# Kernel optimization log

Hardware: AMD Instinct MI355X
Metric: run time of the kernel (lower is better)

Reference implementation:

```python
import jax, jax.numpy as jnp
import numpy as np

N_HEADS = 16

def _apply_rope(x, cos, sin):
    # x: [B, S, H, D]; cos/sin: [S, D//2]
    B, S, H, D = x.shape
    half = D // 2
    x1, x2 = x[..., :half], x[..., half:]
    c = cos[:S, None, :]  # [S, 1, half] -> broadcast over heads
    s = sin[:S, None, :]
    o1 = x1 * c - x2 * s
    o2 = x1 * s + x2 * c
    return jnp.concatenate([o1, o2], axis=-1).astype(x.dtype)


def setup_inputs() -> dict:
    key = jax.random.key(0)
    ks = jax.random.split(key, 6)
    B, S, dim = 2, 2048, 2048
    head_dim = dim // N_HEADS
    half = head_dim // 2
    x = jax.random.normal(ks[0], (B, S, dim), dtype=jnp.float32)
    # real RoPE tables (theta=10000)
    inv_freq = 1.0 / (10000.0 ** (np.arange(0, half, dtype=np.float32) / half))
    t = np.arange(S, dtype=np.float32)
    freqs = np.outer(t, inv_freq)  # [S, half]
    cos = jnp.asarray(np.cos(freqs), dtype=jnp.float32)
    sin = jnp.asarray(np.sin(freqs), dtype=jnp.float32)
    scale = 0.02
    wq = jax.random.normal(ks[1], (dim, dim), dtype=jnp.float32) * scale
    wk = jax.random.normal(ks[2], (dim, dim), dtype=jnp.float32) * scale
    wv = jax.random.normal(ks[3], (dim, dim), dtype=jnp.float32) * scale
    wo = jax.random.normal(ks[4], (dim, dim), dtype=jnp.float32) * scale
    return {"x": x, "cos": cos, "sin": sin, "wq": wq, "wk": wk, "wv": wv, "wo": wo}


def reference(x, cos, sin, wq, wk, wv, wo):
    B, S, dim = x.shape
    H = N_HEADS
    Dh = dim // H
    # QKV projections (nn.Linear: x @ W.T)
    q = (x @ wq.T).reshape(B, S, H, Dh)
    k = (x @ wk.T).reshape(B, S, H, Dh)
    v = (x @ wv.T).reshape(B, S, H, Dh)
    q = _apply_rope(q, cos, sin)
    k = _apply_rope(k, cos, sin)
    # causal attention (flash_attn_func with causal=True, dropout 0 in eval)
    scores = jnp.einsum('bqhd,bkhd->bhqk', q, k) / jnp.sqrt(jnp.asarray(Dh, x.dtype))
    causal = jnp.tril(jnp.ones((S, S), dtype=bool))
    scores = jnp.where(causal, scores, jnp.asarray(-1e30, x.dtype))
    attn = jax.nn.softmax(scores, axis=-1)
    out = jnp.einsum('bhqk,bkhd->bqhd', attn, v).reshape(B, S, dim)
    return out @ wo.T
```

## Files before the change

kernel.cpp:

```cpp
#include <hip/hip_runtime.h>

typedef short short8 __attribute__((ext_vector_type(8)));
typedef float f32x4 __attribute__((ext_vector_type(4)));
typedef unsigned short ushort_t;

__device__ __forceinline__ unsigned short f2bf(float f){
  unsigned int u = __builtin_bit_cast(unsigned int, f);
  u += 0x7FFFu + ((u >> 16) & 1u);
  return (unsigned short)(u >> 16);
}
__device__ __forceinline__ float bf2f(unsigned short u){
  return __builtin_bit_cast(float, ((unsigned int)u) << 16);
}
__device__ __forceinline__ void gload_lds16(const void* g, void* l){
  __builtin_amdgcn_global_load_lds((const __attribute__((address_space(1))) unsigned int*)g,
                                   (__attribute__((address_space(3))) unsigned int*)l, 16, 0, 0);
}

__global__ __launch_bounds__(256) void cast_bf16_kernel(const float* __restrict__ in,
                                                        ushort_t* __restrict__ out, long n4){
  long i = (long)blockIdx.x*256 + threadIdx.x;
  if (i >= n4) return;
  const float4 v = reinterpret_cast<const float4*>(in)[i];
  ushort4 o; o.x=f2bf(v.x); o.y=f2bf(v.y); o.z=f2bf(v.z); o.w=f2bf(v.w);
  reinterpret_cast<ushort4*>(out)[i] = o;
}

__global__ __launch_bounds__(256) void cast4_bf16_kernel(const float* __restrict__ w0, const float* __restrict__ w1,
                                                         const float* __restrict__ w2, const float* __restrict__ w3,
                                                         ushort_t* __restrict__ o0, ushort_t* __restrict__ o1,
                                                         ushort_t* __restrict__ o2, ushort_t* __restrict__ o3,
                                                         long n4){
  long i = (long)blockIdx.x*256 + threadIdx.x;
  if (i >= n4) return;
  const float* in; ushort_t* out;
  switch (blockIdx.y){
    case 0: in = w0; out = o0; break;
    case 1: in = w1; out = o1; break;
    case 2: in = w2; out = o2; break;
    default: in = w3; out = o3; break;
  }
  const float4 v = reinterpret_cast<const float4*>(in)[i];
  ushort4 o; o.x=f2bf(v.x); o.y=f2bf(v.y); o.z=f2bf(v.z); o.w=f2bf(v.w);
  reinterpret_cast<ushort4*>(out)[i] = o;
}

__global__ __launch_bounds__(256) void rope2_kernel(ushort_t* __restrict__ Qs,
                                                    ushort_t* __restrict__ Ks,
                                                    const float* __restrict__ cosb,
                                                    const float* __restrict__ sinb){
  long idx = (long)blockIdx.x*256 + threadIdx.x;
  ushort_t* X = blockIdx.y ? Ks : Qs;
  const float scale = blockIdx.y ? 1.0f : 0.08838834764831845f;
  int dq = (int)(idx & 15);
  long rest = idx >> 4;
  int h = (int)(rest & 15); rest >>= 4;
  int s = (int)(rest & 2047);
  int b = (int)(rest >> 11);
  long base = ((long)(b*2048 + s))*2048 + h*128;
  int d0 = dq*4;
  ushort4 x1 = *(const ushort4*)&X[base + d0];
  ushort4 x2 = *(const ushort4*)&X[base + 64 + d0];
  float4 cc = *(const float4*)&cosb[s*64 + d0];
  float4 ss = *(const float4*)&sinb[s*64 + d0];
  ushort4 o1, o2;
  { float a=bf2f(x1.x), bb=bf2f(x2.x); o1.x=f2bf((a*cc.x-bb*ss.x)*scale); o2.x=f2bf((a*ss.x+bb*cc.x)*scale); }
  { float a=bf2f(x1.y), bb=bf2f(x2.y); o1.y=f2bf((a*cc.y-bb*ss.y)*scale); o2.y=f2bf((a*ss.y+bb*cc.y)*scale); }
  { float a=bf2f(x1.z), bb=bf2f(x2.z); o1.z=f2bf((a*cc.z-bb*ss.z)*scale); o2.z=f2bf((a*ss.z+bb*cc.z)*scale); }
  { float a=bf2f(x1.w), bb=bf2f(x2.w); o1.w=f2bf((a*cc.w-bb*ss.w)*scale); o2.w=f2bf((a*ss.w+bb*cc.w)*scale); }
  *(ushort4*)&X[base + d0] = o1;
  *(ushort4*)&X[base + 64 + d0] = o2;
}


#define LDA4(P, QM, KH) do{ \
  _Pragma("unroll") for (int i_ = 0; i_ < 4; ++i_) \
    af[i_] = *(const short8*)&lA[(P)*16384 + ((QM)*128 + aRowBase + i_*16)*64 + ((KH)? sw1 : sw0)]; }while(0)

#define LDB4K(P, KH) do{ \
  _Pragma("unroll") for (int j_ = 0; j_ < 4; ++j_) \
    bfr[KH][j_] = *(const short8*)&lB[(P)*16384 + (((j_>>1)*128) + bRowBase + (j_&1)*16)*64 + ((KH)? sw1 : sw0)]; }while(0)

#define STAGE_A(P, QM, T) do{ \
  gload_lds16(aS0 + (long)(QM)*64*K + (long)(T)*64, &lA[(P)*16384 + (QM)*8192 + tid*8]); \
  gload_lds16(aS1 + (long)(QM)*64*K + (long)(T)*64, &lA[(P)*16384 + (QM)*8192 + 4096 + tid*8]); }while(0)

#define STAGE_B(P, QN, T) do{ \
  gload_lds16(bS0 + (long)(QN)*32*K + (long)(T)*64, &lB[(P)*16384 + (QN)*8192 + tid*8]); \
  gload_lds16(bS1 + (long)(QN)*32*K + (long)(T)*64, &lB[(P)*16384 + (QN)*8192 + 4096 + tid*8]); }while(0)

#define MFK(QM, KH) do{ \
  __builtin_amdgcn_s_setprio(1); \
  _Pragma("unroll") for (int i_ = 0; i_ < 4; ++i_) \
    _Pragma("unroll") for (int j_ = 0; j_ < 4; ++j_) \
      acc[(QM)*4+i_][j_] = __builtin_amdgcn_mfma_f32_16x16x32_bf16(af[i_], bfr[KH][j_], acc[(QM)*4+i_][j_], 0, 0, 0); \
  __builtin_amdgcn_s_setprio(0); }while(0)

#define WAITC(MORE) do{ \
  if (MORE) asm volatile("s_waitcnt vmcnt(4)" ::: "memory"); \
  else      asm volatile("s_waitcnt vmcnt(0)" ::: "memory"); }while(0)

#define PHX(RD, STG, WT, QM, KH) do{ \
  RD; \
  STG; \
  WT; \
  __builtin_amdgcn_s_barrier(); \
  asm volatile("" ::: "memory"); \
  MFK(QM, KH); \
  __builtin_amdgcn_s_barrier(); \
  asm volatile("" ::: "memory"); }while(0)

__global__ __launch_bounds__(512, 2) void gemm_qkv_8ph(const ushort_t* __restrict__ A,
                                                       const ushort_t* __restrict__ Bw,
                                                       ushort_t* __restrict__ Cq,
                                                       ushort_t* __restrict__ Ck,
                                                       ushort_t* __restrict__ Vt,
                                                       int MT, int K){
  __shared__ ushort_t lA[32768];
  __shared__ ushort_t lB[32768];
  const int tid = threadIdx.x;
  const int lane = tid & 63, wid = tid >> 6;
  const int g = lane >> 4, c = lane & 15;
  const int wm = wid >> 2, wn = wid & 3;

  const int nwg = (int)gridDim.x, cpx = nwg >> 3;
  int sw = (blockIdx.x & 7)*cpx + (blockIdx.x >> 3);
  const long m0 = (long)(sw % MT)*256;
  const long n0 = (long)(sw / MT)*256;

  const int prl0 = tid >> 3, q1 = 512 + tid, prl1 = q1 >> 3;
  const int sl0 = ((tid & 7) ^ (prl0 & 7)) * 8;
  const int sl1 = ((q1 & 7) ^ (prl1 & 7)) * 8;
  const int rowA0 = ((prl0 >> 6)*128) + (prl0 & 63);
  const int rowA1 = ((prl1 >> 6)*128) + (prl1 & 63);
  const int rowB0 = ((prl0 >> 5)*64) + (prl0 & 31);
  const int rowB1 = ((prl1 >> 5)*64) + (prl1 & 31);
  const ushort_t* aS0 = A + (m0 + rowA0)*K + sl0;
  const ushort_t* aS1 = A + (m0 + rowA1)*K + sl1;
  const ushort_t* bS0 = Bw + (n0 + rowB0)*K + sl0;
  const ushort_t* bS1 = Bw + (n0 + rowB1)*K + sl1;

  const int sw0 = (g ^ (c & 7)) * 8;
  const int sw1 = ((4 + g) ^ (c & 7)) * 8;
  const int aRowBase = wm*64 + c;
  const int bRowBase = wn*32 + c;

  f32x4 acc[8][4] = {};
  short8 af[4], bfr[2][4];
  const int NI = K >> 7;

  STAGE_A(0, 0, 0); STAGE_B(0, 0, 0);
  STAGE_A(0, 1, 0); STAGE_B(0, 1, 0);
  STAGE_A(1, 0, 1); STAGE_B(1, 0, 1);
  asm volatile("s_waitcnt vmcnt(4)" ::: "memory");
  __builtin_amdgcn_s_barrier();
  asm volatile("" ::: "memory");

  for (int j = 0; j < NI; ++j){
    const int t = 2*j;
    const bool more = (j + 1 < NI);
    PHX(LDB4K(0,0); LDA4(0,0,0), STAGE_A(1, 1, t+1),            ((void)0),   0, 0);
    PHX(LDB4K(0,1); LDA4(0,0,1), STAGE_B(1, 1, t+1),            ((void)0),   0, 1);
    PHX(LDA4(0,1,0),             if(more){STAGE_A(0, 0, t+2);}, ((void)0),   1, 0);
    PHX(LDA4(0,1,1),             if(more){STAGE_B(0, 0, t+2);}, WAITC(more), 1, 1);
    PHX(LDB4K(1,0); LDA4(1,0,0), if(more){STAGE_A(0, 1, t+2);}, ((void)0),   0, 0);
    PHX(LDB4K(1,1); LDA4(1,0,1), if(more){STAGE_B(0, 1, t+2);}, ((void)0),   0, 1);
    PHX(LDA4(1,1,0),             if(more){STAGE_A(1, 0, t+3);}, ((void)0),   1, 0);
    PHX(LDA4(1,1,1),             if(more){STAGE_B(1, 0, t+3);}, WAITC(more), 1, 1);
  }

  const long rbase = m0 + wm*128 + g*4;
  const long cbase = n0 + wn*64 + c;
  const int third = (int)(n0 >> 11);
  if (third < 2){
    ushort_t* dst = (third == 0) ? Cq : Ck;
    const long csub = cbase - (long)third*2048;
#pragma unroll
    for (int mi = 0; mi < 8; ++mi)
#pragma unroll
      for (int ni = 0; ni < 4; ++ni){
        long off = (rbase + mi*16)*2048 + csub + ni*16;
#pragma unroll
        for (int r = 0; r < 4; ++r)
          dst[off + (long)r*2048] = f2bf(acc[mi][ni][r]);
      }
  } else {
#pragma unroll
    for (int mi = 0; mi < 8; ++mi){
      const long row = rbase + mi*16;
      const long s = row & 2047, bb = row >> 11;
#pragma unroll
      for (int ni = 0; ni < 4; ++ni){
        long hd = cbase + ni*16 - 4096;
        long vaddr = ((bb*16 + (hd >> 7))*128 + (hd & 127))*2048 + s;
        ushort4 o4;
        o4.x = f2bf(acc[mi][ni][0]); o4.y = f2bf(acc[mi][ni][1]);
        o4.z = f2bf(acc[mi][ni][2]); o4.w = f2bf(acc[mi][ni][3]);
        *(ushort4*)&Vt[vaddr] = o4;
      }
    }
  }
}

__global__ __launch_bounds__(256) void gemm_nt_lds(const ushort_t* __restrict__ A,
                                                   const ushort_t* __restrict__ B,
                                                   float* __restrict__ C,
                                                   int M, int N, int K){
  const int tid = threadIdx.x;
  const int l = tid & 63;
  const int g = l >> 4, c = l & 15;
  const int w = tid >> 6, wr = w >> 1, wc = w & 1;
  const long m0 = (long)blockIdx.x*128, n0 = (long)blockIdx.y*128;
  __shared__ ushort_t lds_a[128*32];
  __shared__ ushort_t lds_b[128*32];
  f32x4 acc[4][4] = {};
  const int q1 = tid, q2 = 256 + tid;
  const ushort_t* a1 = A + (m0 + (q1>>2))*(long)K + (q1&3)*8;
  const ushort_t* a2 = A + (m0 + (q2>>2))*(long)K + (q2&3)*8;
  const ushort_t* b1 = B + (n0 + (q1>>2))*(long)K + (q1&3)*8;
  const ushort_t* b2 = B + (n0 + (q2>>2))*(long)K + (q2&3)*8;
  for (int k0 = 0; k0 < K; k0 += 32){
    __syncthreads();
    gload_lds16(a1 + k0, &lds_a[q1*8]);
    gload_lds16(a2 + k0, &lds_a[q2*8]);
    gload_lds16(b1 + k0, &lds_b[q1*8]);
    gload_lds16(b2 + k0, &lds_b[q2*8]);
    __syncthreads();
    short8 af[4], bf[4];
#pragma unroll
    for (int i = 0; i < 4; ++i) af[i] = *(const short8*)&lds_a[(wr*64 + i*16 + c)*32 + g*8];
#pragma unroll
    for (int j = 0; j < 4; ++j) bf[j] = *(const short8*)&lds_b[(wc*64 + j*16 + c)*32 + g*8];
#pragma unroll
    for (int i = 0; i < 4; ++i)
#pragma unroll
      for (int j = 0; j < 4; ++j)
        acc[i][j] = __builtin_amdgcn_mfma_f32_16x16x32_bf16(af[i], bf[j], acc[i][j], 0, 0, 0);
  }
#pragma unroll
  for (int i = 0; i < 4; ++i)
#pragma unroll
    for (int j = 0; j < 4; ++j)
#pragma unroll
      for (int r = 0; r < 4; ++r)
        C[(m0 + wr*64 + i*16 + g*4 + r)*(long)N + n0 + wc*64 + j*16 + c] = acc[i][j][r];
}

__global__ __launch_bounds__(256) void attn_kernel(const ushort_t* __restrict__ Q,
                                                   const ushort_t* __restrict__ Kr,
                                                   const ushort_t* __restrict__ Vt,
                                                   ushort_t* __restrict__ O){
  const int tid = threadIdx.x;
  const int l = tid & 63, w = tid >> 6;
  const int g = l >> 4, c = l & 15;
  const int bh = blockIdx.x;
  const int qt = (int)gridDim.y - 1 - (int)blockIdx.y;
  const int b = bh >> 4, h = bh & 15;
  const int q0 = qt * 64;
  const int qw0 = q0 + w * 16;
  const int nt = qt + 1;

  __shared__ ushort_t k_lds[2][64*128];
  __shared__ ushort_t v_lds[2][128*64];
  __shared__ ushort_t p_lds[4][16*72];

  short8 qf[4];
  const long qbase = ((long)(b*2048 + qw0 + c))*2048 + h*128 + g*8;
#pragma unroll
  for (int ds = 0; ds < 4; ++ds) qf[ds] = *(const short8*)(Q + qbase + ds*32);

  const ushort_t* ksrc[4]; const ushort_t* vsrc[4];
  int kof[4], vof[4];
#pragma unroll
  for (int i = 0; i < 4; ++i){
    int q = i*256 + tid;
    int r = q >> 4, j = q & 15;
    ksrc[i] = Kr + ((long)(b*2048 + r))*2048 + h*128 + (j ^ (r & 7))*8;
    kof[i] = q*8;
    int d = q >> 3, jj = q & 7;
    vsrc[i] = Vt + ((long)(bh*128 + d))*2048 + (jj ^ (d & 7))*8;
    vof[i] = q*8;
  }

  f32x4 o[8] = {};
  float m = -1e30f, lsum = 0.f;
  const int sw = (c & 7) << 3;

#pragma unroll
  for (int i = 0; i < 4; ++i) gload_lds16(ksrc[i], &k_lds[0][kof[i]]);
#pragma unroll
  for (int i = 0; i < 4; ++i) gload_lds16(vsrc[i], &v_lds[0][vof[i]]);
  __syncthreads();

  for (int t = 0; t < nt; ++t){
    const int p = t & 1;
    if (t + 1 < nt){
#pragma unroll
      for (int i = 0; i < 4; ++i)
        gload_lds16(ksrc[i] + (long)(t+1)*64*2048, &k_lds[p^1][kof[i]]);
#pragma unroll
      for (int i = 0; i < 4; ++i)
        gload_lds16(vsrc[i] + (t+1)*64, &v_lds[p^1][vof[i]]);
    }
    const int kv0 = t*64;

    f32x4 s[4] = {};
    __builtin_amdgcn_s_setprio(1);
#pragma unroll
    for (int t4 = 0; t4 < 4; ++t4){
      const int row = 16*t4 + c;
#pragma unroll
      for (int ds = 0; ds < 4; ++ds){
        short8 kf = *(const short8*)&k_lds[p][(row*128 + ds*32 + g*8) ^ sw];
        s[t4] = __builtin_amdgcn_mfma_f32_16x16x32_bf16(kf, qf[ds], s[t4], 0, 0, 0);
      }
    }
    __builtin_amdgcn_s_setprio(0);
    if (kv0 + 63 > qw0){
      const int qg = qw0 + c;
#pragma unroll
      for (int t4 = 0; t4 < 4; ++t4)
#pragma unroll
        for (int r = 0; r < 4; ++r)
          if (kv0 + 16*t4 + 4*g + r > qg) s[t4][r] = -1e30f;
    }
    float tm = -1e30f;
#pragma unroll
    for (int t4 = 0; t4 < 4; ++t4)
      tm = fmaxf(tm, fmaxf(fmaxf(s[t4][0], s[t4][1]), fmaxf(s[t4][2], s[t4][3])));
    tm = fmaxf(tm, __shfl_xor(tm, 16, 64));
    tm = fmaxf(tm, __shfl_xor(tm, 32, 64));
    if (!__all(tm <= m + 8.f)){
      float mn = fmaxf(m, tm);
      float al = __expf(m - mn);
      m = mn;
      lsum *= al;
      float alr[4];
#pragma unroll
      for (int r = 0; r < 4; ++r) alr[r] = __shfl(al, 4*g + r, 64);
#pragma unroll
      for (int dt = 0; dt < 8; ++dt)
#pragma unroll
        for (int r = 0; r < 4; ++r) o[dt][r] *= alr[r];
    }
    float ps = 0.f;
#pragma unroll
    for (int t4 = 0; t4 < 4; ++t4)
#pragma unroll
      for (int r = 0; r < 4; ++r){ float pex = __expf(s[t4][r] - m); s[t4][r] = pex; ps += pex; }
    ps += __shfl_xor(ps, 16, 64);
    ps += __shfl_xor(ps, 32, 64);
    lsum += ps;
#pragma unroll
    for (int t4 = 0; t4 < 4; ++t4){
      uint2 pw;
      pw.x = (unsigned)f2bf(s[t4][0]) | ((unsigned)f2bf(s[t4][1]) << 16);
      pw.y = (unsigned)f2bf(s[t4][2]) | ((unsigned)f2bf(s[t4][3]) << 16);
      *reinterpret_cast<uint2*>(&p_lds[w][c*72 + 16*t4 + 4*g]) = pw;
    }
    __builtin_amdgcn_s_setprio(1);
#pragma unroll
    for (int kc = 0; kc < 2; ++kc){
      short8 pf = *(const short8*)&p_lds[w][c*72 + 32*kc + 8*g];
#pragma unroll
      for (int dt = 0; dt < 8; ++dt){
        short8 vf = *(const short8*)&v_lds[p][(((16*dt + c)*64) + kc*32 + g*8) ^ sw];
        o[dt] = __builtin_amdgcn_mfma_f32_16x16x32_bf16(pf, vf, o[dt], 0, 0, 0);
      }
    }
    __builtin_amdgcn_s_setprio(0);
    __syncthreads();
  }

  float inv = 1.f / lsum;
  float invr[4];
#pragma unroll
  for (int r = 0; r < 4; ++r) invr[r] = __shfl(inv, 4*g + r, 64);
  const long obase = ((long)(b*2048 + qw0 + g*4))*2048 + h*128 + c;
#pragma unroll
  for (int dt = 0; dt < 8; ++dt)
#pragma unroll
    for (int r = 0; r < 4; ++r)
      O[obase + (long)r*2048 + dt*16] = f2bf(o[dt][r] * invr[r]);
}

extern "C" void kernel_launch(void* const* d_in, const int* in_sizes, int n_in,
                              void* d_out, int out_size, void* d_ws, size_t ws_size,
                              hipStream_t stream){
  const float* x    = (const float*)d_in[0];
  const float* cosb = (const float*)d_in[1];
  const float* sinb = (const float*)d_in[2];
  const float* wq   = (const float*)d_in[3];
  const float* wk   = (const float*)d_in[4];
  const float* wv   = (const float*)d_in[5];
  const float* wo   = (const float*)d_in[6];
  float* out = (float*)d_out;

  const int S = 2048, DIM = 2048;
  const long MN = 4096;

  char* ws = (char*)d_ws;
  ushort_t* xb     = (ushort_t*)(ws);
  ushort_t* wqkvb  = (ushort_t*)(ws + (16l<<20));
  ushort_t* wob    = (ushort_t*)(ws + (40l<<20));
  ushort_t* qstage = (ushort_t*)(ws + (48l<<20));
  ushort_t* kstage = (ushort_t*)(ws + (64l<<20));
  ushort_t* attnb  = (ushort_t*)(ws + (80l<<20));
  ushort_t* vt     = (ushort_t*)(ws + (96l<<20));

  const long xn4 = MN*DIM/4, wn4 = (long)DIM*DIM/4;
  cast_bf16_kernel<<<(int)((xn4+255)/256), 256, 0, stream>>>(x, xb, xn4);
  cast4_bf16_kernel<<<dim3((int)((wn4+255)/256), 4), 256, 0, stream>>>(
      wq, wk, wv, wo,
      wqkvb, wqkvb + 4194304, wqkvb + 8388608, wob, wn4);

  gemm_qkv_8ph<<<(MN/256)*(6144/256), 512, 0, stream>>>(
      xb, wqkvb, qstage, kstage, vt, (int)(MN/256), DIM);

  const int ropeBlocks = (2*2048*16*16)/256;
  rope2_kernel<<<dim3(ropeBlocks, 2), 256, 0, stream>>>(qstage, kstage, cosb, sinb);
  attn_kernel<<<dim3(32, S/64), 256, 0, stream>>>(qstage, kstage, vt, attnb);
  gemm_nt_lds<<<dim3(MN/128, DIM/128), 256, 0, stream>>>(attnb, wob, out, (int)MN, DIM, DIM);
}
```

Measured before the change: 301.0 us.

## Switch QKV GEMM to 32x32x16 MFMA with double-buffered register fragments

Rewrites the fused QKV projection GEMM's inner loop to use 32x32x16 bf16 MFMA tiles instead of 16x16x32. This changes the LDS swizzle, the fragment loads and the accumulator layout to f32x16. LDS fragment reads now alternate between even and odd register sets so that the next phase's reads are issued before the current MFMA batch. The last iteration is peeled so the loop needs no conditional staging, and the epilogue store indexing is rewritten for the new accumulator layout. Register pressure rises and the new swizzle risks LDS bank conflicts or indexing errors.

New measurement: 312.2 us. 3.7% more time.

```diff
diff --git a/kernel.cpp b/kernel.cpp
--- a/kernel.cpp
+++ b/kernel.cpp
@@ -2,6 +2,7 @@
 
 typedef short short8 __attribute__((ext_vector_type(8)));
 typedef float f32x4 __attribute__((ext_vector_type(4)));
+typedef float f32x16 __attribute__((ext_vector_type(16)));
 typedef unsigned short ushort_t;
 
 __device__ __forceinline__ unsigned short f2bf(float f){
@@ -73,13 +74,19 @@
 }
 
 
-#define LDA4(P, QM, KH) do{ \
-  _Pragma("unroll") for (int i_ = 0; i_ < 4; ++i_) \
-    af[i_] = *(const short8*)&lA[(P)*16384 + ((QM)*128 + aRowBase + i_*16)*64 + ((KH)? sw1 : sw0)]; }while(0)
-
-#define LDB4K(P, KH) do{ \
-  _Pragma("unroll") for (int j_ = 0; j_ < 4; ++j_) \
-    bfr[KH][j_] = *(const short8*)&lB[(P)*16384 + (((j_>>1)*128) + bRowBase + (j_&1)*16)*64 + ((KH)? sw1 : sw0)]; }while(0)
+#define LDA_SET(DST, P, MQ, KH) do{ \
+  _Pragma("unroll") for (int mt2 = 0; mt2 < 2; ++mt2) \
+    _Pragma("unroll") for (int k2 = 0; k2 < 2; ++k2){ \
+      int R_ = (MQ)*128 + wm*64 + mt2*32 + l31; \
+      int sl_ = (4*(KH) + 2*k2 + hh) ^ fl; \
+      DST[mt2][k2] = *(const short8*)&lA[(P)*16384 + R_*64 + sl_*8]; } }while(0)
+
+#define LDB_SET(DST, P, KH) do{ \
+  _Pragma("unroll") for (int nt2 = 0; nt2 < 2; ++nt2) \
+    _Pragma("unroll") for (int k2 = 0; k2 < 2; ++k2){ \
+      int R_ = nt2*128 + wn*32 + l31; \
+      int sl_ = (4*(KH) + 2*k2 + hh) ^ fl; \
+      DST[nt2][k2] = *(const short8*)&lB[(P)*16384 + R_*64 + sl_*8]; } }while(0)
 
 #define STAGE_A(P, QM, T) do{ \
   gload_lds16(aS0 + (long)(QM)*64*K + (long)(T)*64, &lA[(P)*16384 + (QM)*8192 + tid*8]); \
@@ -89,26 +96,16 @@
   gload_lds16(bS0 + (long)(QN)*32*K + (long)(T)*64, &lB[(P)*16384 + (QN)*8192 + tid*8]); \
   gload_lds16(bS1 + (long)(QN)*32*K + (long)(T)*64, &lB[(P)*16384 + (QN)*8192 + 4096 + tid*8]); }while(0)
 
-#define MFK(QM, KH) do{ \
+#define MFMA8(AS, BS, MQ) do{ \
   __builtin_amdgcn_s_setprio(1); \
-  _Pragma("unroll") for (int i_ = 0; i_ < 4; ++i_) \
-    _Pragma("unroll") for (int j_ = 0; j_ < 4; ++j_) \
-      acc[(QM)*4+i_][j_] = __builtin_amdgcn_mfma_f32_16x16x32_bf16(af[i_], bfr[KH][j_], acc[(QM)*4+i_][j_], 0, 0, 0); \
+  _Pragma("unroll") for (int mt2 = 0; mt2 < 2; ++mt2) \
+    _Pragma("unroll") for (int nt2 = 0; nt2 < 2; ++nt2) \
+      _Pragma("unroll") for (int k2 = 0; k2 < 2; ++k2) \
+        acc[2*(MQ)+mt2][nt2] = __builtin_amdgcn_mfma_f32_32x32x16_bf16(AS[mt2][k2], BS[nt2][k2], acc[2*(MQ)+mt2][nt2], 0, 0, 0); \
   __builtin_amdgcn_s_setprio(0); }while(0)
 
-#define WAITC(MORE) do{ \
-  if (MORE) asm volatile("s_waitcnt vmcnt(4)" ::: "memory"); \
-  else      asm volatile("s_waitcnt vmcnt(0)" ::: "memory"); }while(0)
-
-#define PHX(RD, STG, WT, QM, KH) do{ \
-  RD; \
-  STG; \
-  WT; \
-  __builtin_amdgcn_s_barrier(); \
-  asm volatile("" ::: "memory"); \
-  MFK(QM, KH); \
-  __builtin_amdgcn_s_barrier(); \
-  asm volatile("" ::: "memory"); }while(0)
+#define BAR() do{ __builtin_amdgcn_s_barrier(); asm volatile("" ::: "memory"); }while(0)
+#define VM(N) asm volatile("s_waitcnt vmcnt(" #N ")" ::: "memory")
 
 __global__ __launch_bounds__(512, 2) void gemm_qkv_8ph(const ushort_t* __restrict__ A,
                                                        const ushort_t* __restrict__ Bw,
@@ -120,85 +117,97 @@
   __shared__ ushort_t lB[32768];
   const int tid = threadIdx.x;
   const int lane = tid & 63, wid = tid >> 6;
-  const int g = lane >> 4, c = lane & 15;
+  const int l31 = lane & 31, hh = lane >> 5;
   const int wm = wid >> 2, wn = wid & 3;
+  const int fl = (lane & 7) ^ ((l31 >> 3) & 3);
 
   const int nwg = (int)gridDim.x, cpx = nwg >> 3;
   int sw = (blockIdx.x & 7)*cpx + (blockIdx.x >> 3);
   const long m0 = (long)(sw % MT)*256;
   const long n0 = (long)(sw / MT)*256;
 
-  const int prl0 = tid >> 3, q1 = 512 + tid, prl1 = q1 >> 3;
-  const int sl0 = ((tid & 7) ^ (prl0 & 7)) * 8;
-  const int sl1 = ((q1 & 7) ^ (prl1 & 7)) * 8;
-  const int rowA0 = ((prl0 >> 6)*128) + (prl0 & 63);
-  const int rowA1 = ((prl1 >> 6)*128) + (prl1 & 63);
-  const int rowB0 = ((prl0 >> 5)*64) + (prl0 & 31);
-  const int rowB1 = ((prl1 >> 5)*64) + (prl1 & 31);
-  const ushort_t* aS0 = A + (m0 + rowA0)*K + sl0;
-  const ushort_t* aS1 = A + (m0 + rowA1)*K + sl1;
-  const ushort_t* bS0 = Bw + (n0 + rowB0)*K + sl0;
-  const ushort_t* bS1 = Bw + (n0 + rowB1)*K + sl1;
-
-  const int sw0 = (g ^ (c & 7)) * 8;
-  const int sw1 = ((4 + g) ^ (c & 7)) * 8;
-  const int aRowBase = wm*64 + c;
-  const int bRowBase = wn*32 + c;
-
-  f32x4 acc[8][4] = {};
-  short8 af[4], bfr[2][4];
+  const int Rl = tid >> 3;
+  const int ft = (Rl & 7) ^ ((Rl >> 3) & 3);
+  const int sl = ((tid & 7) ^ ft) * 8;
+  const int rowA0 = Rl, rowA1 = 128 + Rl;
+  const int rowB0 = (Rl >> 5)*64 + (Rl & 31), rowB1 = 128 + rowB0;
+  const ushort_t* aS0 = A + (m0 + rowA0)*K + sl;
+  const ushort_t* aS1 = A + (m0 + rowA1)*K + sl;
+  const ushort_t* bS0 = Bw + (n0 + rowB0)*K + sl;
+  const ushort_t* bS1 = Bw + (n0 + rowB1)*K + sl;
+
+  f32x16 acc[4][2] = {};
+  short8 aE[2][2], aO[2][2], bE[2][2], bO[2][2];
   const int NI = K >> 7;
 
   STAGE_A(0, 0, 0); STAGE_B(0, 0, 0);
   STAGE_A(0, 1, 0); STAGE_B(0, 1, 0);
   STAGE_A(1, 0, 1); STAGE_B(1, 0, 1);
-  asm volatile("s_waitcnt vmcnt(4)" ::: "memory");
-  __builtin_amdgcn_s_barrier();
-  asm volatile("" ::: "memory");
-
-  for (int j = 0; j < NI; ++j){
+  VM(4);
+  BAR();
+  LDA_SET(aE, 0, 0, 0); LDB_SET(bE, 0, 0);
+
+  for (int j = 0; j < NI-1; ++j){
     const int t = 2*j;
-    const bool more = (j + 1 < NI);
-    PHX(LDB4K(0,0); LDA4(0,0,0), STAGE_A(1, 1, t+1),            ((void)0),   0, 0);
-    PHX(LDB4K(0,1); LDA4(0,0,1), STAGE_B(1, 1, t+1),            ((void)0),   0, 1);
-    PHX(LDA4(0,1,0),             if(more){STAGE_A(0, 0, t+2);}, ((void)0),   1, 0);
-    PHX(LDA4(0,1,1),             if(more){STAGE_B(0, 0, t+2);}, WAITC(more), 1, 1);
-    PHX(LDB4K(1,0); LDA4(1,0,0), if(more){STAGE_A(0, 1, t+2);}, ((void)0),   0, 0);
-    PHX(LDB4K(1,1); LDA4(1,0,1), if(more){STAGE_B(0, 1, t+2);}, ((void)0),   0, 1);
-    PHX(LDA4(1,1,0),             if(more){STAGE_A(1, 0, t+3);}, ((void)0),   1, 0);
-    PHX(LDA4(1,1,1),             if(more){STAGE_B(1, 0, t+3);}, WAITC(more), 1, 1);
-  }
-
-  const long rbase = m0 + wm*128 + g*4;
-  const long cbase = n0 + wn*64 + c;
+     LDA_SET(aO, 0, 1, 0);                    STAGE_A(1, 1, t+1); BAR(); MFMA8(aE, bE, 0); BAR();
+     LDA_SET(aE, 0, 0, 1); LDB_SET(bO, 0, 1); STAGE_B(1, 1, t+1); BAR(); MFMA8(aO, bE, 1); BAR();
+     LDA_SET(aO, 0, 1, 1);                    STAGE_A(0, 0, t+2); BAR(); MFMA8(aE, bO, 0); BAR();
+     VM(2);
+            LDA_SET(aE, 1, 0, 0); LDB_SET(bE, 1, 0); STAGE_B(0, 0, t+2); BAR(); MFMA8(aO, bO, 1); BAR();
+     LDA_SET(aO, 1, 1, 0);                    STAGE_A(0, 1, t+2); BAR(); MFMA8(aE, bE, 0); BAR();
+     LDA_SET(aE, 1, 0, 1); LDB_SET(bO, 1, 1); STAGE_B(0, 1, t+2); BAR(); MFMA8(aO, bE, 1); BAR();
+     LDA_SET(aO, 1, 1, 1);                    STAGE_A(1, 0, t+3); BAR(); MFMA8(aE, bO, 0); BAR();
+     VM(2);
+            LDA_SET(aE, 0, 0, 0); LDB_SET(bE, 0, 0); STAGE_B(1, 0, t+3); BAR(); MFMA8(aO, bO, 1); BAR();
+  }
+  {
+    const int t = 2*(NI-1);
+     LDA_SET(aO, 0, 1, 0);                    STAGE_A(1, 1, t+1); BAR(); MFMA8(aE, bE, 0); BAR();
+     LDA_SET(aE, 0, 0, 1); LDB_SET(bO, 0, 1); STAGE_B(1, 1, t+1); BAR(); MFMA8(aO, bE, 1); BAR();
+     LDA_SET(aO, 0, 1, 1);                                        BAR(); MFMA8(aE, bO, 0); BAR();
+     VM(0);
+            LDA_SET(aE, 1, 0, 0); LDB_SET(bE, 1, 0);                     BAR(); MFMA8(aO, bO, 1); BAR();
+     LDA_SET(aO, 1, 1, 0);                                        BAR(); MFMA8(aE, bE, 0); BAR();
+     LDA_SET(aE, 1, 0, 1); LDB_SET(bO, 1, 1);                     BAR(); MFMA8(aO, bE, 1); BAR();
+     LDA_SET(aO, 1, 1, 1);                                        BAR(); MFMA8(aE, bO, 0); BAR();
+                                                                  BAR(); MFMA8(aO, bO, 1); BAR();
+  }
+
   const int third = (int)(n0 >> 11);
   if (third < 2){
     ushort_t* dst = (third == 0) ? Cq : Ck;
-    const long csub = cbase - (long)third*2048;
-#pragma unroll
-    for (int mi = 0; mi < 8; ++mi)
-#pragma unroll
-      for (int ni = 0; ni < 4; ++ni){
-        long off = (rbase + mi*16)*2048 + csub + ni*16;
-#pragma unroll
-        for (int r = 0; r < 4; ++r)
-          dst[off + (long)r*2048] = f2bf(acc[mi][ni][r]);
+    const long csub = n0 - (long)third*2048 + wn*64 + l31;
+#pragma unroll
+    for (int mti = 0; mti < 4; ++mti)
+#pragma unroll
+      for (int nt = 0; nt < 2; ++nt){
+        const long col = csub + nt*32;
+#pragma unroll
+        for (int q = 0; q < 4; ++q){
+          const long row0 = m0 + wm*128 + mti*32 + 8*q + 4*hh;
+#pragma unroll
+          for (int rq = 0; rq < 4; ++rq)
+            dst[(row0 + rq)*2048 + col] = f2bf(acc[mti][nt][4*q + rq]);
+        }
       }
   } else {
-#pragma unroll
-    for (int mi = 0; mi < 8; ++mi){
-      const long row = rbase + mi*16;
-      const long s = row & 2047, bb = row >> 11;
-#pragma unroll
-      for (int ni = 0; ni < 4; ++ni){
-        long hd = cbase + ni*16 - 4096;
-        long vaddr = ((bb*16 + (hd >> 7))*128 + (hd & 127))*2048 + s;
-        ushort4 o4;
-        o4.x = f2bf(acc[mi][ni][0]); o4.y = f2bf(acc[mi][ni][1]);
-        o4.z = f2bf(acc[mi][ni][2]); o4.w = f2bf(acc[mi][ni][3]);
-        *(ushort4*)&Vt[vaddr] = o4;
+    const long hdb = n0 - 4096 + wn*64 + l31;
+#pragma unroll
+    for (int mti = 0; mti < 4; ++mti)
+#pragma unroll
+      for (int nt = 0; nt < 2; ++nt){
+        const long hd = hdb + nt*32;
+        const long dbase = ((hd >> 7)*128 + (hd & 127))*2048;
+#pragma unroll
+        for (int q = 0; q < 4; ++q){
+          const long row0 = m0 + wm*128 + mti*32 + 8*q + 4*hh;
+          const long s = row0 & 2047, bb = row0 >> 11;
+          ushort4 o4;
+          o4.x = f2bf(acc[mti][nt][4*q + 0]); o4.y = f2bf(acc[mti][nt][4*q + 1]);
+          o4.z = f2bf(acc[mti][nt][4*q + 2]); o4.w = f2bf(acc[mti][nt][4*q + 3]);
+          *(ushort4*)&Vt[bb*4194304 + dbase + s] = o4;
+        }
       }
-    }
   }
 }
 
```
